# Kernel tuning notes

Measured on AMD Instinct MI355X. Metric: run time of the kernel, lower is better.

The kernel has to match this reference:

```python
import jax, jax.numpy as jnp
import numpy as np

RES0 = 128
SCALES = [1, 2, 4, 8]
OUT_DIM = 32
PLANES = [(0, 1), (0, 2), (1, 2)]  # itertools.combinations(range(3), 2)


def _bilinear(grid, cx, cy):
    """grid: [C,H,W]; cx maps to W, cy maps to H; coords in [-1,1].
    Matches F.grid_sample(mode='bilinear', align_corners=True, padding_mode='border')."""
    C, H, W = grid.shape
    x = jnp.clip((cx + 1.0) * 0.5 * (W - 1), 0.0, W - 1)
    y = jnp.clip((cy + 1.0) * 0.5 * (H - 1), 0.0, H - 1)
    x0 = jnp.floor(x)
    y0 = jnp.floor(y)
    wx = (x - x0)[:, None]  # [N,1]
    wy = (y - y0)[:, None]
    x0i = x0.astype(jnp.int32)
    y0i = y0.astype(jnp.int32)
    x1i = jnp.minimum(x0i + 1, W - 1)
    y1i = jnp.minimum(y0i + 1, H - 1)
    g00 = grid[:, y0i, x0i].T  # [N,C]
    g01 = grid[:, y0i, x1i].T
    g10 = grid[:, y1i, x0i].T
    g11 = grid[:, y1i, x1i].T
    top = g00 * (1.0 - wx) + g01 * wx
    bot = g10 * (1.0 - wx) + g11 * wx
    return top * (1.0 - wy) + bot * wy  # [N,C]


def _interpolate_ms_features(x, ms_grids):
    feats = []
    for scale_grids in ms_grids:  # fixed 4 scales
        interp_space = 1.0
        for ci, (a, b) in enumerate(PLANES):  # fixed 3 planes
            interp_space = interp_space * _bilinear(scale_grids[ci], x[:, a], x[:, b])
        feats.append(interp_space)
    return jnp.concatenate(feats, axis=-1)  # [N, 4*OUT_DIM]


def _mlp(f, w0, w1, w2):
    h = jax.nn.relu(f @ w0)
    h = jax.nn.relu(h @ w1)
    return h @ w2  # [N,1], linear output (tcnn, bias-free)


def setup_inputs() -> dict:
    key = jax.random.key(0)
    ks = jax.random.split(key, 16)
    N = 1_000_000
    inp = {"x": jax.random.uniform(ks[0], (N, 3), jnp.float32, -1.0, 1.0)}
    i = 1
    for s, mult in enumerate(SCALES):
        R = RES0 * mult
        for p in range(3):
            # nn.init.uniform_(a=0.1, b=0.5)
            inp[f"g{s}p{p}"] = jax.random.uniform(ks[i], (OUT_DIM, R, R), jnp.float32, 0.1, 0.5)
            i += 1
    F = OUT_DIM * len(SCALES)
    inp["w0"] = jax.random.normal(ks[13], (F, 64), jnp.float32) / np.sqrt(F).astype(np.float32)
    inp["w1"] = jax.random.normal(ks[14], (64, 64), jnp.float32) / 8.0
    inp["w2"] = jax.random.normal(ks[15], (64, 1), jnp.float32) / 8.0
    return inp


def reference(x, g0p0, g0p1, g0p2, g1p0, g1p1, g1p2, g2p0, g2p1, g2p2,
              g3p0, g3p1, g3p2, w0, w1, w2):
    ms_grids = [(g0p0, g0p1, g0p2), (g1p0, g1p1, g1p2),
                (g2p0, g2p1, g2p2), (g3p0, g3p1, g3p2)]
    features = _interpolate_ms_features(x, ms_grids)
    return _mlp(features, w0, w1, w2)
```

## Files before the change

kernel.cpp:

```cpp
#include <hip/hip_runtime.h>
#include <cstddef>


typedef unsigned short ushort_t;
typedef unsigned int uint_t;
typedef __bf16 bf16x8 __attribute__((ext_vector_type(8)));
typedef float f32x4 __attribute__((ext_vector_type(4)));

struct KParams {
  const float* x;
  const void* g[12];
  const float* w0;
  const float* w1;
  const float* w2;
  const ushort_t* w0T;
  const ushort_t* w1T;
  float* out;
  int N;
};

struct TP3 {
  const float* src[3];
  ushort_t* dst[3];
  int RR;
};

__device__ __forceinline__ ushort_t f32_to_bf16_rne(float f) {
  uint_t u = __float_as_uint(f);
  u = (u + 0x7FFFu + ((u >> 16) & 1u)) >> 16;
  return (ushort_t)u;
}

__global__ __launch_bounds__(256) void transpose3(TP3 tp) {
  const float* __restrict__ in = tp.src[blockIdx.y];
  ushort_t* __restrict__ out = tp.dst[blockIdx.y];
  const int RR = tp.RR;
  __shared__ float tile[32][65];
  const int p0 = blockIdx.x * 64;
  {
    const int tp_ = threadIdx.x & 63;
    const int tc = threadIdx.x >> 6;
#pragma unroll
    for (int cc = 0; cc < 8; ++cc) {
      const int c = cc * 4 + tc;
      tile[c][tp_] = in[(size_t)c * RR + p0 + tp_];
    }
  }
  __syncthreads();
  {
    const int c2 = threadIdx.x & 15;
    const int tq = threadIdx.x >> 4;
    uint_t* o32 = (uint_t*)out;
#pragma unroll
    for (int pp = 0; pp < 4; ++pp) {
      const int pos = pp * 16 + tq;
      const uint_t lo = f32_to_bf16_rne(tile[2 * c2 + 0][pos]);
      const uint_t hi = f32_to_bf16_rne(tile[2 * c2 + 1][pos]);
      o32[(size_t)(p0 + pos) * 16 + c2] = lo | (hi << 16);
    }
  }
}

__global__ __launch_bounds__(256) void prep_weights(
    const float* __restrict__ w0, const float* __restrict__ w1,
    ushort_t* __restrict__ w0T, ushort_t* __restrict__ w1T) {
  const int t = threadIdx.x;
  for (int i = t; i < 128 * 64; i += 256) {
    const int k = i >> 6, n = i & 63;
    w0T[n * 128 + k] = f32_to_bf16_rne(w0[i]);
  }
  for (int i = t; i < 64 * 64; i += 256) {
    const int k = i >> 6, n = i & 63;
    w1T[n * 64 + k] = f32_to_bf16_rne(w1[i]);
  }
}

__global__ __launch_bounds__(512, 8) void kplanes_fused_mfma(KParams P) {
  __shared__ float arena[10240];
  int* ci = (int*)arena;
  float* cf = arena;
  uint_t* feat32 = (uint_t*)(arena + 6144);
  float* px = arena + 6144;

  const int t = threadIdx.x;
  const int blk0 = blockIdx.x * 64;

  if (t < 192) {
    const int p = t / 3, e = t - p * 3;
    int Pi = blk0 + p;
    if (Pi >= P.N) Pi = P.N - 1;
    px[t] = P.x[3 * Pi + e];
  }
  __syncthreads();

  for (int task = t; task < 768; task += 512) {
    const int pt = task & 63;
    const int sm = task >> 6;
    const int pl = sm >> 2;
    const int s = sm & 3;
    const float cx = (pl == 2) ? px[pt * 3 + 1] : px[pt * 3 + 0];
    const float cy = (pl == 0) ? px[pt * 3 + 1] : px[pt * 3 + 2];
    const int R = 128 << s;
    const float Rm1 = (float)(R - 1);
    const float u = fminf(fmaxf((cx + 1.0f) * 0.5f * Rm1, 0.0f), Rm1);
    const float v = fminf(fmaxf((cy + 1.0f) * 0.5f * Rm1, 0.0f), Rm1);
    const float fx0 = floorf(u), fy0 = floorf(v);
    const int x0 = (int)fx0, y0 = (int)fy0;
    const int x1 = min(x0 + 1, R - 1), y1 = min(y0 + 1, R - 1);
    const int base = task * 8;
    int4 o4;
    o4.x = y0 * R + x0;
    o4.y = y0 * R + x1;
    o4.z = y1 * R + x0;
    o4.w = y1 * R + x1;
    *(int4*)(ci + base) = o4;
    cf[base + 4] = u - fx0;
    cf[base + 5] = v - fy0;
  }
  __syncthreads();

  const int pt = t >> 3;
  const int q = t & 7;
  const int cg = q & 3;
  const int sh = q >> 2;
  uint_t* prow = feat32 + pt * 64;
  const int wxor = (pt & 7) << 2;

#pragma unroll
  for (int j = 0; j < 2; ++j) {
    const int s = 2 * j + sh;
    float f[8];
#pragma unroll
    for (int c = 0; c < 8; ++c) f[c] = 1.0f;

#pragma unroll
    for (int pl = 0; pl < 3; ++pl) {
      const int base = ((pl * 4 + s) * 64 + pt) * 8;
      const int4 o4 = *(const int4*)(ci + base);
      const float wx = cf[base + 4], wy = cf[base + 5];
      const float w11 = wx * wy;
      const float w10 = wy - w11;
      const float w01 = wx - w11;
      const float w00 = 1.0f - wx - w10;
      const ushort_t* gp = (const ushort_t*)P.g[s * 3 + pl];
      const uint4 qa = *(const uint4*)(gp + (size_t)o4.x * 32 + cg * 8);
      const uint4 qb = *(const uint4*)(gp + (size_t)o4.y * 32 + cg * 8);
      const uint4 qc = *(const uint4*)(gp + (size_t)o4.z * 32 + cg * 8);
      const uint4 qd = *(const uint4*)(gp + (size_t)o4.w * 32 + cg * 8);
#define CH2(dA, dB, dC, dD, i0, i1)                                \
  {                                                                \
    float rl = __uint_as_float((dD) << 16) * w11;                  \
    rl = fmaf(__uint_as_float((dC) << 16), w10, rl);               \
    rl = fmaf(__uint_as_float((dB) << 16), w01, rl);               \
    rl = fmaf(__uint_as_float((dA) << 16), w00, rl);               \
    f[i0] *= rl;                                                   \
    float rh = __uint_as_float((dD)&0xFFFF0000u) * w11;            \
    rh = fmaf(__uint_as_float((dC)&0xFFFF0000u), w10, rh);         \
    rh = fmaf(__uint_as_float((dB)&0xFFFF0000u), w01, rh);         \
    rh = fmaf(__uint_as_float((dA)&0xFFFF0000u), w00, rh);         \
    f[i1] *= rh;                                                   \
  }
      CH2(qa.x, qb.x, qc.x, qd.x, 0, 1)
      CH2(qa.y, qb.y, qc.y, qd.y, 2, 3)
      CH2(qa.z, qb.z, qc.z, qd.z, 4, 5)
      CH2(qa.w, qb.w, qc.w, qd.w, 6, 7)
#undef CH2
    }

    uint_t d0, d1, d2, d3;
    asm("v_cvt_pk_bf16_f32 %0, %1, %2" : "=v"(d0) : "v"(f[0]), "v"(f[1]));
    asm("v_cvt_pk_bf16_f32 %0, %1, %2" : "=v"(d1) : "v"(f[2]), "v"(f[3]));
    asm("v_cvt_pk_bf16_f32 %0, %1, %2" : "=v"(d2) : "v"(f[4]), "v"(f[5]));
    asm("v_cvt_pk_bf16_f32 %0, %1, %2" : "=v"(d3) : "v"(f[6]), "v"(f[7]));
    uint4 dv;
    dv.x = d0; dv.y = d1; dv.z = d2; dv.w = d3;
    *(uint4*)(prow + ((s * 16 + cg * 4) ^ wxor)) = dv;
  }
  __syncthreads();

  ushort_t* lds_h = (ushort_t*)arena;
  float(*oparts)[64] = (float(*)[64])(arena + 2048);

  const int w = __builtin_amdgcn_readfirstlane(t >> 6);
  const int mt = w & 3;
  const int nt0 = (w >> 2) << 1;
  const int ln = t & 15;
  const int lq = (t >> 4) & 3;
  const int arow = mt * 16 + ln;

  const uint_t* farow = feat32 + arow * 64;
  const int axor = (arow & 7) << 2;
  f32x4 acc0a = {0.f, 0.f, 0.f, 0.f}, acc0b = {0.f, 0.f, 0.f, 0.f};
  const ushort_t* w0a = P.w0T + (nt0 * 16 + ln) * 128 + lq * 8;
  const ushort_t* w0b = w0a + 16 * 128;
#pragma unroll
  for (int kt = 0; kt < 4; ++kt) {
    const bf16x8 aF = *(const bf16x8*)(farow + ((kt * 16 + lq * 4) ^ axor));
    const bf16x8 bFa = *(const bf16x8*)(w0a + kt * 32);
    const bf16x8 bFb = *(const bf16x8*)(w0b + kt * 32);
    acc0a = __builtin_amdgcn_mfma_f32_16x16x32_bf16(aF, bFa, acc0a, 0, 0, 0);
    acc0b = __builtin_amdgcn_mfma_f32_16x16x32_bf16(aF, bFb, acc0b, 0, 0, 0);
  }

#pragma unroll
  for (int i = 0; i < 2; ++i) {
    const f32x4 a = i ? acc0b : acc0a;
    const int col = (nt0 + i) * 16 + ln;
#pragma unroll
    for (int jj = 0; jj < 4; ++jj) {
      const float v = fmaxf(a[jj], 0.0f);
      uint_t dv;
      asm("v_cvt_pk_bf16_f32 %0, %1, %2" : "=v"(dv) : "v"(v), "v"(v));
      const int r = mt * 16 + lq * 4 + jj;
      lds_h[r * 64 + (col ^ ((r & 7) << 3))] = (ushort_t)dv;
    }
  }
  __syncthreads();

  const ushort_t* hrow = lds_h + arow * 64;
  const int hxor = (arow & 7) << 3;
  f32x4 acc1a = {0.f, 0.f, 0.f, 0.f}, acc1b = {0.f, 0.f, 0.f, 0.f};
  const ushort_t* w1a = P.w1T + (nt0 * 16 + ln) * 64 + lq * 8;
  const ushort_t* w1b = w1a + 16 * 64;
#pragma unroll
  for (int kt = 0; kt < 2; ++kt) {
    const bf16x8 aF = *(const bf16x8*)(hrow + ((kt * 32 + lq * 8) ^ hxor));
    const bf16x8 bFa = *(const bf16x8*)(w1a + kt * 32);
    const bf16x8 bFb = *(const bf16x8*)(w1b + kt * 32);
    acc1a = __builtin_amdgcn_mfma_f32_16x16x32_bf16(aF, bFa, acc1a, 0, 0, 0);
    acc1b = __builtin_amdgcn_mfma_f32_16x16x32_bf16(aF, bFb, acc1b, 0, 0, 0);
  }

  const float w2a = P.w2[nt0 * 16 + ln];
  const float w2b = P.w2[(nt0 + 1) * 16 + ln];
  float part[4];
#pragma unroll
  for (int jj = 0; jj < 4; ++jj)
    part[jj] = fmaxf(acc1a[jj], 0.f) * w2a + fmaxf(acc1b[jj], 0.f) * w2b;
#pragma unroll
  for (int jj = 0; jj < 4; ++jj) {
    part[jj] += __shfl_xor(part[jj], 1);
    part[jj] += __shfl_xor(part[jj], 2);
    part[jj] += __shfl_xor(part[jj], 4);
    part[jj] += __shfl_xor(part[jj], 8);
  }
  if (ln == 0) {
#pragma unroll
    for (int jj = 0; jj < 4; ++jj)
      oparts[w >> 2][mt * 16 + lq * 4 + jj] = part[jj];
  }
  __syncthreads();

  if (t < 64) {
    const int Po = blk0 + t;
    if (Po < P.N) P.out[Po] = oparts[0][t] + oparts[1][t];
  }
}

__global__ __launch_bounds__(512, 8) void kplanes_fused_scalar(KParams P) {
  __shared__ float fl[64][130];
  const int t = threadIdx.x;
  const int pg = t >> 3;
  const int sub = t & 7;
  const int blk0 = blockIdx.x * 64;

  int Pi = blk0 + pg;
  if (Pi >= P.N) Pi = P.N - 1;
  const float c0 = P.x[3 * Pi + 0];
  const float c1 = P.x[3 * Pi + 1];
  const float c2 = P.x[3 * Pi + 2];

  float feat[4][4];
#pragma unroll
  for (int s = 0; s < 4; ++s)
#pragma unroll
    for (int c = 0; c < 4; ++c) feat[s][c] = 1.0f;

#pragma unroll
  for (int s = 0; s < 4; ++s) {
    const int R = 128 << s;
    const int RR = R * R;
#pragma unroll
    for (int pl = 0; pl < 3; ++pl) {
      const float cx = (pl == 2) ? c1 : c0;
      const float cy = (pl == 0) ? c1 : c2;
      const float Rm1 = (float)(R - 1);
      const float u = fminf(fmaxf((cx + 1.0f) * 0.5f * Rm1, 0.0f), Rm1);
      const float v = fminf(fmaxf((cy + 1.0f) * 0.5f * Rm1, 0.0f), Rm1);
      const float fx0 = floorf(u), fy0 = floorf(v);
      const float wx = u - fx0, wy = v - fy0;
      const int x0 = (int)fx0, y0 = (int)fy0;
      const int x1 = min(x0 + 1, R - 1), y1 = min(y0 + 1, R - 1);
      const float w11 = wx * wy;
      const float w10 = wy - w11;
      const float w01 = wx - w11;
      const float w00 = 1.0f - wx - w10;
      const float* gp = (const float*)P.g[s * 3 + pl];
      const int i00 = y0 * R + x0, i01 = y0 * R + x1;
      const int i10 = y1 * R + x0, i11 = y1 * R + x1;
#pragma unroll
      for (int c = 0; c < 4; ++c) {
        const size_t cb = (size_t)(sub * 4 + c) * RR;
        feat[s][c] *= gp[cb + i00] * w00 + gp[cb + i01] * w01 +
                      gp[cb + i10] * w10 + gp[cb + i11] * w11;
      }
    }
  }

#pragma unroll
  for (int s = 0; s < 4; ++s)
#pragma unroll
    for (int c = 0; c < 4; ++c)
      fl[pg][s * 32 + sub * 4 + c] = feat[s][c];
  __syncthreads();

  const int p = t & 63;
  const int g = __builtin_amdgcn_readfirstlane(t >> 6);

  const float* w0c = P.w0 + g * 8;
  float part[8];
#pragma unroll
  for (int jj = 0; jj < 8; ++jj) part[jj] = 0.0f;
#pragma unroll 16
  for (int k = 0; k < 128; ++k) {
    const float f = fl[p][k];
#pragma unroll
    for (int jj = 0; jj < 8; ++jj)
      part[jj] = fmaf(f, w0c[(size_t)k * 64 + jj], part[jj]);
  }
  __syncthreads();
#pragma unroll
  for (int jj = 0; jj < 8; ++jj)
    fl[p][g * 8 + jj] = fmaxf(part[jj], 0.0f);
  __syncthreads();

  const float* w1c = P.w1 + g * 8;
  float h1[8];
#pragma unroll
  for (int jj = 0; jj < 8; ++jj) h1[jj] = 0.0f;
#pragma unroll 16
  for (int k = 0; k < 64; ++k) {
    const float a = fl[p][k];
#pragma unroll
    for (int jj = 0; jj < 8; ++jj)
      h1[jj] = fmaf(a, w1c[(size_t)k * 64 + jj], h1[jj]);
  }

  const float* w2c = P.w2 + g * 8;
  float o = 0.0f;
#pragma unroll
  for (int jj = 0; jj < 8; ++jj)
    o = fmaf(fmaxf(h1[jj], 0.0f), w2c[jj], o);

  __syncthreads();
  ((float*)fl)[g * 64 + p] = o;
  __syncthreads();

  if (t < 64) {
    const int Po = blk0 + t;
    if (Po < P.N) {
      const float* f0 = (const float*)fl;
      float r = 0.0f;
#pragma unroll
      for (int j = 0; j < 8; ++j) r += f0[j * 64 + t];
      P.out[Po] = r;
    }
  }
}

extern "C" void kernel_launch(void* const* d_in, const int* in_sizes, int n_in,
                              void* d_out, int out_size, void* d_ws, size_t ws_size,
                              hipStream_t stream) {
  KParams P;
  P.x = (const float*)d_in[0];
  P.w0 = (const float*)d_in[13];
  P.w1 = (const float*)d_in[14];
  P.w2 = (const float*)d_in[15];
  P.out = (float*)d_out;
  const int N = in_sizes[0] / 3;
  P.N = N;

  size_t need = 0;
  for (int s = 0; s < 4; ++s) {
    const size_t R = (size_t)(128 << s);
    need += 3ull * 32ull * R * R * sizeof(ushort_t);
  }
  const size_t walign = (need + 255) & ~(size_t)255;
  const size_t wbytes = (size_t)(64 * 128 + 64 * 64) * sizeof(ushort_t);

  const int nblk = (N + 63) / 64;
  if (ws_size >= walign + wbytes) {
    ushort_t* w = (ushort_t*)d_ws;
    size_t off = 0;
    for (int s = 0; s < 4; ++s) {
      const int R = 128 << s;
      const int RR = R * R;
      TP3 tp;
      tp.RR = RR;
      for (int pl = 0; pl < 3; ++pl) {
        tp.src[pl] = (const float*)d_in[1 + s * 3 + pl];
        tp.dst[pl] = w + off;
        P.g[s * 3 + pl] = w + off;
        off += (size_t)32 * RR;
      }
      dim3 grid(RR / 64, 3);
      transpose3<<<grid, 256, 0, stream>>>(tp);
    }
    ushort_t* w0T = (ushort_t*)((char*)d_ws + walign);
    ushort_t* w1T = w0T + 64 * 128;
    P.w0T = w0T;
    P.w1T = w1T;
    prep_weights<<<1, 256, 0, stream>>>(P.w0, P.w1, w0T, w1T);
    kplanes_fused_mfma<<<nblk, 512, 0, stream>>>(P);
  } else {
    for (int k = 0; k < 12; ++k) P.g[k] = (const void*)d_in[1 + k];
    P.w0T = nullptr;
    P.w1T = nullptr;
    kplanes_fused_scalar<<<nblk, 512, 0, stream>>>(P);
  }
}
```

Baseline: 730.0 us.

## Sort query points by Morton key and remap blocks per XCD for grid locality

Adds a counting sort of input points into 32^3 Morton buckets (histogram, scan, scatter) so that each 64-point block samples spatially nearby texels, which should improve cache hit rates on the gathered plane grids. The fused MFMA kernel is templated to read the sorted coordinates and scatter its outputs back through the index array. It also remaps block IDs so that consecutive sorted blocks land on the same XCD and share its L2. This adds three extra kernels and a memset, atomics in the histogram and scatter, and a scattered final write.

```diff
diff --git a/kernel.cpp b/kernel.cpp
--- a/kernel.cpp
+++ b/kernel.cpp
@@ -6,6 +6,8 @@
 typedef unsigned int uint_t;
 typedef __bf16 bf16x8 __attribute__((ext_vector_type(8)));
 typedef float f32x4 __attribute__((ext_vector_type(4)));
+
+#define NBUCKET 32768
 
 struct KParams {
   const float* x;
@@ -15,6 +17,8 @@
   const float* w2;
   const ushort_t* w0T;
   const ushort_t* w1T;
+  const float* xs;
+  const int* sidx;
   float* out;
   int N;
 };
@@ -75,6 +79,67 @@
   }
 }
 
+__device__ __forceinline__ uint_t spread5(uint_t v) {
+  return (v & 1u) | ((v & 2u) << 2) | ((v & 4u) << 4) | ((v & 8u) << 6) |
+         ((v & 16u) << 8);
+}
+__device__ __forceinline__ uint_t morton_key(const float* __restrict__ x,
+                                             int i) {
+  const float a = x[3 * i + 0];
+  const float b = x[3 * i + 1];
+  const float c = x[3 * i + 2];
+  const uint_t ua = (uint_t)fminf(fmaxf((a + 1.0f) * 16.0f, 0.0f), 31.0f);
+  const uint_t ub = (uint_t)fminf(fmaxf((b + 1.0f) * 16.0f, 0.0f), 31.0f);
+  const uint_t uc = (uint_t)fminf(fmaxf((c + 1.0f) * 16.0f, 0.0f), 31.0f);
+  return spread5(ua) | (spread5(ub) << 1) | (spread5(uc) << 2);
+}
+
+__global__ __launch_bounds__(256) void sort_hist(const float* __restrict__ x,
+                                                 uint_t* __restrict__ cnt,
+                                                 int N) {
+  const int i = blockIdx.x * 256 + threadIdx.x;
+  if (i < N) atomicAdd(&cnt[morton_key(x, i)], 1u);
+}
+
+__global__ __launch_bounds__(1024) void sort_scan(uint_t* __restrict__ cnt) {
+  __shared__ uint_t s[1024];
+  const int t = threadIdx.x;
+  const int base = t * 32;
+  uint_t p = 0;
+#pragma unroll
+  for (int e = 0; e < 32; ++e) p += cnt[base + e];
+  s[t] = p;
+  __syncthreads();
+  for (int off = 1; off < 1024; off <<= 1) {
+    uint_t v = 0;
+    if (t >= off) v = s[t - off];
+    __syncthreads();
+    s[t] += v;
+    __syncthreads();
+  }
+  uint_t running = s[t] - p;
+#pragma unroll
+  for (int e = 0; e < 32; ++e) {
+    const uint_t old = cnt[base + e];
+    cnt[base + e] = running;
+    running += old;
+  }
+}
+
+__global__ __launch_bounds__(256) void sort_scatter(
+    const float* __restrict__ x, uint_t* __restrict__ cnt,
+    int* __restrict__ sidx, float* __restrict__ xs, int N) {
+  const int i = blockIdx.x * 256 + threadIdx.x;
+  if (i >= N) return;
+  const uint_t key = morton_key(x, i);
+  const uint_t pos = atomicAdd(&cnt[key], 1u);
+  sidx[pos] = i;
+  xs[3 * pos + 0] = x[3 * i + 0];
+  xs[3 * pos + 1] = x[3 * i + 1];
+  xs[3 * pos + 2] = x[3 * i + 2];
+}
+
+template <bool SORTED>
 __global__ __launch_bounds__(512, 8) void kplanes_fused_mfma(KParams P) {
   __shared__ float arena[10240];
   int* ci = (int*)arena;
@@ -83,13 +148,29 @@
   float* px = arena + 6144;
 
   const int t = threadIdx.x;
-  const int blk0 = blockIdx.x * 64;
-
-  if (t < 192) {
-    const int p = t / 3, e = t - p * 3;
-    int Pi = blk0 + p;
-    if (Pi >= P.N) Pi = P.N - 1;
-    px[t] = P.x[3 * Pi + e];
+
+  int bid = blockIdx.x;
+  if (SORTED) {
+    const int nblk = gridDim.x;
+    const int q = nblk >> 3, r = nblk & 7;
+    const int xcd = bid & 7, idx = bid >> 3;
+    bid = (xcd < r ? xcd * (q + 1) : r * (q + 1) + (xcd - r) * q) + idx;
+  }
+  const int blk0 = bid * 64;
+
+  if (SORTED) {
+    if (t < 192) {
+      int idx = blk0 * 3 + t;
+      if (idx >= 3 * P.N) idx = 3 * P.N - 3 + (t % 3);
+      px[t] = P.xs[idx];
+    }
+  } else {
+    if (t < 192) {
+      const int p = t / 3, e = t - p * 3;
+      int Pi = blk0 + p;
+      if (Pi >= P.N) Pi = P.N - 1;
+      px[t] = P.x[3 * Pi + e];
+    }
   }
   __syncthreads();
 
@@ -253,7 +334,13 @@
 
   if (t < 64) {
     const int Po = blk0 + t;
-    if (Po < P.N) P.out[Po] = oparts[0][t] + oparts[1][t];
+    if (Po < P.N) {
+      const float r = oparts[0][t] + oparts[1][t];
+      if (SORTED)
+        P.out[P.sidx[Po]] = r;
+      else
+        P.out[Po] = r;
+    }
   }
 }
 
@@ -379,6 +466,8 @@
   P.out = (float*)d_out;
   const int N = in_sizes[0] / 3;
   P.N = N;
+  P.xs = nullptr;
+  P.sidx = nullptr;
 
   size_t need = 0;
   for (int s = 0; s < 4; ++s) {
@@ -387,6 +476,11 @@
   }
   const size_t walign = (need + 255) & ~(size_t)255;
   const size_t wbytes = (size_t)(64 * 128 + 64 * 64) * sizeof(ushort_t);
+  const size_t cntoff = (walign + wbytes + 255) & ~(size_t)255;
+  const size_t cntbytes = (size_t)NBUCKET * 4;
+  const size_t sidxoff = cntoff + cntbytes;
+  const size_t xsoff = (sidxoff + (size_t)N * 4 + 255) & ~(size_t)255;
+  const size_t total_sorted = xsoff + (size_t)N * 12;
 
   const int nblk = (N + 63) / 64;
   if (ws_size >= walign + wbytes) {
@@ -411,7 +505,22 @@
     P.w0T = w0T;
     P.w1T = w1T;
     prep_weights<<<1, 256, 0, stream>>>(P.w0, P.w1, w0T, w1T);
-    kplanes_fused_mfma<<<nblk, 512, 0, stream>>>(P);
+
+    if (ws_size >= total_sorted) {
+      uint_t* cnt = (uint_t*)((char*)d_ws + cntoff);
+      int* sidx = (int*)((char*)d_ws + sidxoff);
+      float* xs = (float*)((char*)d_ws + xsoff);
+      hipMemsetAsync(cnt, 0, cntbytes, stream);
+      const int pblk = (N + 255) / 256;
+      sort_hist<<<pblk, 256, 0, stream>>>(P.x, cnt, N);
+      sort_scan<<<1, 1024, 0, stream>>>(cnt);
+      sort_scatter<<<pblk, 256, 0, stream>>>(P.x, cnt, sidx, xs, N);
+      P.xs = xs;
+      P.sidx = sidx;
+      kplanes_fused_mfma<true><<<nblk, 512, 0, stream>>>(P);
+    } else {
+      kplanes_fused_mfma<false><<<nblk, 512, 0, stream>>>(P);
+    }
   } else {
     for (int k = 0; k < 12; ++k) P.g[k] = (const void*)d_in[1 + k];
     P.w0T = nullptr;
```

New measurement: 656.6 us. 10.1% less time.
